# Performance work log

Hardware: AMD Instinct MI355X
Metric: run time of the kernel (lower is better)

## Reference

```python
import jax, jax.numpy as jnp
import numpy as np

N, T, F = 4096, 24, 16          # nodes, seq_len, in_features
H = 128                          # temporal_hidden
NH, DO = 4, 32                   # gat num_heads, gat out_features (NH*DO == H)
SEM, PH = 64, 32                 # semantic hidden, predictor hidden
SLOPE = 0.2                      # leaky_relu negative slope
ADJ_P = 0.01                     # adjacency density


def setup_inputs() -> dict:
    key = jax.random.key(0)
    ks = jax.random.split(key, 40)
    f32 = jnp.float32

    def rn(k, shape, s=0.02):
        return jax.random.normal(k, shape, f32) * s

    features = jax.random.normal(ks[0], (N, T, F), f32)
    pos_adj = (jax.random.uniform(ks[1], (N, N)) < ADJ_P).astype(f32)
    neg_adj = (jax.random.uniform(ks[2], (N, N)) < ADJ_P).astype(f32)

    inp = dict(features=features, pos_adj=pos_adj, neg_adj=neg_adj)
    # GRU (torch layout: W_ih [3H,F], W_hh [3H,H], gate order r,z,n)
    inp['gru_Wih'] = rn(ks[3], (3 * H, F), 1.0 / np.sqrt(H))
    inp['gru_Whh'] = rn(ks[4], (3 * H, H), 1.0 / np.sqrt(H))
    inp['gru_bih'] = rn(ks[5], (3 * H,), 1.0 / np.sqrt(H))
    inp['gru_bhh'] = rn(ks[6], (3 * H,), 1.0 / np.sqrt(H))
    # GAT params (linear weights stored [in, out] so we use x @ W)
    i = 7
    for pre in ('pos', 'neg'):
        inp[pre + '_W'] = rn(ks[i], (H, NH * DO)); i += 1
        inp[pre + '_u'] = rn(ks[i], (NH, DO, 1), 1.0); i += 1
        inp[pre + '_v'] = rn(ks[i], (NH, DO, 1), 1.0); i += 1
        inp[pre + '_b'] = rn(ks[i], (1, NH * DO)); i += 1
        inp[pre + '_pW'] = rn(ks[i], (H, NH * DO)); i += 1
        inp[pre + '_pb'] = jnp.zeros((NH * DO,), f32)
    inp['self_W'] = rn(ks[i], (H, H)); i += 1
    inp['self_b'] = jnp.zeros((H,), f32)
    inp['mpos_W'] = rn(ks[i], (NH * DO, H)); i += 1
    inp['mpos_b'] = jnp.zeros((H,), f32)
    inp['mneg_W'] = rn(ks[i], (NH * DO, H)); i += 1
    inp['mneg_b'] = jnp.zeros((H,), f32)
    inp['sem_W1'] = rn(ks[i], (H, SEM)); i += 1
    inp['sem_b1'] = jnp.zeros((SEM,), f32)
    inp['sem_W2'] = rn(ks[i], (SEM, 1)); i += 1
    inp['pred_W1'] = rn(ks[i], (H, PH)); i += 1
    inp['pred_b1'] = jnp.zeros((PH,), f32)
    inp['pred_W2'] = rn(ks[i], (PH, 1)); i += 1
    inp['pred_b2'] = jnp.zeros((1,), f32)
    return inp


def _gru_last(x, Wih, Whh, bih, bhh):
    # x: [N, T, F] -> last hidden state [N, H]
    gi_all = jnp.einsum('ntf,gf->tng', x, Wih) + bih  # precompute input gates [T,N,3H]
    h0 = jnp.zeros((x.shape[0], Whh.shape[1]), x.dtype)

    def step(h, gi):
        gh = h @ Whh.T + bhh
        ir, iz, in_ = jnp.split(gi, 3, axis=-1)
        hr, hz, hn = jnp.split(gh, 3, axis=-1)
        r = jax.nn.sigmoid(ir + hr)
        z = jax.nn.sigmoid(iz + hz)
        n = jnp.tanh(in_ + r * hn)
        return (1.0 - z) * n + z * h, None

    h, _ = jax.lax.scan(step, h0, gi_all)
    return h


def _gat(x, adj, W, u, v, b, pW, pb):
    sup = (x @ W).reshape(-1, NH, DO).transpose(1, 0, 2)     # [NH, N, DO]
    f1 = jnp.matmul(sup, u).reshape(NH, 1, -1)               # [NH, 1, N]
    f2 = jnp.matmul(sup, v).reshape(NH, -1, 1)               # [NH, N, 1]
    w = jax.nn.leaky_relu(f1 + f2, SLOPE)                    # [NH, N, N]
    mw = w * adj                                             # mask
    rs = mw.sum(axis=2, keepdims=True)
    rs = jnp.where(rs == 0, jnp.ones_like(rs), rs)
    attn = mw / rs
    out = jnp.matmul(attn, sup).transpose(1, 0, 2).reshape(-1, NH * DO)
    return out + b + x @ pW + pb                             # bias + residual


def _pairnorm_si(x):
    x = x - x.mean(axis=0)
    rn = jnp.sqrt(1e-6 + (x * x).sum(axis=1, keepdims=True))
    return x / rn


def reference(features, pos_adj, neg_adj,
              gru_Wih, gru_Whh, gru_bih, gru_bhh,
              pos_W, pos_u, pos_v, pos_b, pos_pW, pos_pb,
              neg_W, neg_u, neg_v, neg_b, neg_pW, neg_pb,
              self_W, self_b, mpos_W, mpos_b, mneg_W, mneg_b,
              sem_W1, sem_b1, sem_W2,
              pred_W1, pred_b1, pred_W2, pred_b2):
    support = _gru_last(features, gru_Wih, gru_Whh, gru_bih, gru_bhh)  # [N, H]
    pos_sup = _gat(support, pos_adj, pos_W, pos_u, pos_v, pos_b, pos_pW, pos_pb)
    neg_sup = _gat(support, neg_adj, neg_W, neg_u, neg_v, neg_b, neg_pW, neg_pb)
    self_e = support @ self_W + self_b
    pos_e = pos_sup @ mpos_W + mpos_b
    neg_e = neg_sup @ mneg_W + mneg_b
    emb = jnp.stack([self_e, pos_e, neg_e], axis=1)          # [N, 3, H]
    w = jnp.tanh(emb @ sem_W1 + sem_b1) @ sem_W2             # [N, 3, 1]
    beta = jax.nn.softmax(w, axis=1)
    fused = (beta * emb).sum(axis=1)                          # [N, H]
    fused = _pairnorm_si(fused)
    h = jax.nn.relu(fused @ pred_W1 + pred_b1)               # dropout is eval no-op
    out = jax.nn.sigmoid(h @ pred_W2 + pred_b2).squeeze(-1)  # [N]
    return out
```

## Files before the change

### kernel.cpp

```cpp
#include <hip/hip_runtime.h>


#define NN 4096
#define NEG_CSR 1024

typedef unsigned short u16;
typedef unsigned int   u32;
typedef unsigned long long u64;
typedef __attribute__((ext_vector_type(8))) short  short8;
typedef __attribute__((ext_vector_type(4))) float  float4v;

__device__ inline float bf2f(u16 u){ return __uint_as_float(((u32)u)<<16); }
__device__ inline u16 f2bf(float f){
  u32 x = __float_as_uint(f);
  return (u16)((x + 0x7fffu + ((x>>16)&1u))>>16);
}
__device__ inline float ldm(const void* p, int i, int bf){
  return bf ? bf2f(((const u16*)p)[i]) : ((const float*)p)[i];
}
__device__ inline u16 ldm16(const void* p, int i, int bf){
  return bf ? ((const u16*)p)[i] : f2bf(((const float*)p)[i]);
}
__device__ inline float fexp(float x){
  x = fminf(fmaxf(x,-80.f),80.f);
  return __builtin_amdgcn_exp2f(x*1.4426950408889634f);
}
__device__ inline float sigm_fast(float x){
  return __builtin_amdgcn_rcpf(1.f + __builtin_amdgcn_exp2f(-x*1.4426950408889634f));
}
__device__ inline float tanhf_(float x){
  float c = fminf(fmaxf(x,-15.f),15.f);
  float e = __builtin_amdgcn_exp2f(c*2.8853900817779268f);
  return (e-1.f)*__builtin_amdgcn_rcpf(e+1.f);
}
__device__ inline float4v mfma16(short8 a, short8 b, float4v c){
  return __builtin_amdgcn_mfma_f32_16x16x32_bf16(a,b,c,0,0,0);
}
__device__ inline int rdbf(const int* __restrict__ mflag){
  int b=0;
  #pragma unroll
  for (int k=0;k<16;k++) b|=mflag[k];
  return b;
}

__global__ __launch_bounds__(256) void k_detect(const u32* __restrict__ adj,
                                                int* __restrict__ mflag)
{
  __shared__ u32 w4[4];
  const int lane=threadIdx.x&63, wv=threadIdx.x>>6;
  int i = (blockIdx.x*256 + threadIdx.x)*4;
  uint4 v = *(const uint4*)(adj + i);
  u32 acc = (v.x | v.y | v.z | v.w) & 0xFFFFu;
  unsigned long long b = __ballot(acc != 0);
  if (lane==0) w4[wv] = (b!=0);
  __syncthreads();
  if (threadIdx.x==0) mflag[blockIdx.x] = (w4[0]|w4[1]|w4[2]|w4[3]) ? 1 : 0;
}

__global__ __launch_bounds__(256) void k_imp(
  const int* __restrict__ mflag,
  const void* gWih, const void* gWhh, const void* gbih, const void* gbhh,
  const void* posW, const void* posu, const void* posv, const void* posb,
  const void* pospW, const void* pospb,
  const void* negW, const void* negu, const void* negv, const void* negb,
  const void* negpW, const void* negpb,
  const void* selfW, const void* selfb, const void* mposW, const void* mposb,
  const void* mnegW, const void* mnegb,
  const void* semW1, const void* semb1, const void* semW2,
  const void* predW1, const void* predb1, const void* predW2, const void* predb2,
  u16* __restrict__ Wihb, u16* __restrict__ Whhb,
  u16* __restrict__ WT1,  u16* __restrict__ WT2,
  float* __restrict__ cbrz, float* __restrict__ cbin, float* __restrict__ cbhn,
  float* __restrict__ cuv,  float* __restrict__ cgb,  float* __restrict__ csb,
  float* __restrict__ cw1t, float* __restrict__ cb1,  float* __restrict__ cw2,
  float* __restrict__ cpw1t, float* __restrict__ cpb1, float* __restrict__ cpw2,
  float* __restrict__ cpb2, float* __restrict__ meanacc)
{
  const int bf = rdbf(mflag);
  int i = blockIdx.x*256 + threadIdx.x;
  if (i < 6144){ Wihb[i]=ldm16(gWih,i,bf); return; }  i-=6144;
  if (i < 49152){ Whhb[i]=ldm16(gWhh,i,bf); return; } i-=49152;
  if (i < 81920){
    int m=i>>7,k=i&127,sel=m>>7,ml=m&127;
    const void* s = sel==0?posW: sel==1?pospW: sel==2?negW: sel==3?negpW: selfW;
    WT1[i]=ldm16(s,k*128+ml,bf); return;
  } i-=81920;
  if (i < 32768){
    int m=i>>7,k=i&127;
    const void* s = (m<128)? mposW : mnegW;
    WT2[i]=ldm16(s,k*128+(m&127),bf); return;
  } i-=32768;
  if (i < 256){ cbrz[i]=ldm(gbih,i,bf)+ldm(gbhh,i,bf); return; } i-=256;
  if (i < 128){ cbin[i]=ldm(gbih,256+i,bf); return; } i-=128;
  if (i < 128){ cbhn[i]=ldm(gbhh,256+i,bf); return; } i-=128;
  if (i < 512){
    int s=i>>8, rem=i&255, wh=rem>>7, hd=rem&127;
    const void* p = s? (wh? negv:negu) : (wh? posv:posu);
    cuv[i]=ldm(p,hd,bf); return;
  } i-=512;
  if (i < 256){
    int s=i>>7, d=i&127;
    cgb[i]=ldm(s?negb:posb,d,bf)+ldm(s?negpb:pospb,d,bf); return;
  } i-=256;
  if (i < 384){
    int t=i>>7, d=i&127;
    const void* p = t==0? selfb : t==1? mposb : mnegb;
    csb[i]=ldm(p,d,bf); return;
  } i-=384;
  if (i < 8448){
    int c=i/132, k=i-c*132;
    cw1t[i] = (k<128)? ldm(semW1,k*64+c,bf) : 0.f; return;
  } i-=8448;
  if (i < 64){ cb1[i]=ldm(semb1,i,bf); return; } i-=64;
  if (i < 64){ cw2[i]=ldm(semW2,i,bf); return; } i-=64;
  if (i < 4224){
    int c=i/132, k=i-c*132;
    cpw1t[i] = (k<128)? ldm(predW1,k*32+c,bf) : 0.f; return;
  } i-=4224;
  if (i < 32){ cpb1[i]=ldm(predb1,i,bf); return; } i-=32;
  if (i < 32){ cpw2[i]=ldm(predW2,i,bf); return; } i-=32;
  if (i < 1){ cpb2[i]=ldm(predb2,i,bf); return; } i-=1;
  if (i < 128){ meanacc[i]=0.f; return; }
}

__global__ __launch_bounds__(512) void k_gruf(
  const int* __restrict__ mflag, const void* feat,
  const u16* __restrict__ Wihb, const u16* __restrict__ Whhb,
  const float* __restrict__ cbrz, const float* __restrict__ cbin,
  const float* __restrict__ cbhn,
  const u16* __restrict__ WT1, const float* __restrict__ cuv,
  const void* posadj, const void* negadj,
  u16* __restrict__ csri, int* __restrict__ csrc,
  u16* __restrict__ C1b, float* __restrict__ f12)
{
  __shared__ __attribute__((aligned(16))) u16 sh_x[16*392];
  __shared__ __attribute__((aligned(16))) u16 hbuf[2][16*136];
  const int bf = rdbf(mflag);
  const int tid=threadIdx.x, lane=tid&63, wv=tid>>6;

  if (blockIdx.x >= NN/16){
    const int t = (blockIdx.x - NN/16)*8 + wv;
    const int s = (t >= 4096) ? 1 : 0;
    const int i = s ? (t - 4096) : t;
    const void* adj = s? negadj : posadj;
    u64 mask=0;
    if (bf){
      const u16* rp = (const u16*)adj + (size_t)i*4096;
      #pragma unroll
      for (int it=0; it<8; it++){
        const uint4 vv = *(const uint4*)(rp + it*512 + lane*8);
        u32 w[4]={vv.x,vv.y,vv.z,vv.w};
        #pragma unroll
        for (int q=0;q<4;q++){
          if (w[q]&0xffffu) mask |= 1ull<<(it*8+2*q);
          if (w[q]>>16)     mask |= 1ull<<(it*8+2*q+1);
        }
      }
    } else {
      const float* rp = (const float*)adj + (size_t)i*4096;
      #pragma unroll
      for (int it=0; it<16; it++){
        const uint4 vv = *(const uint4*)(rp + it*256 + lane*4);
        if (vv.x) mask |= 1ull<<(it*4+0);
        if (vv.y) mask |= 1ull<<(it*4+1);
        if (vv.z) mask |= 1ull<<(it*4+2);
        if (vv.w) mask |= 1ull<<(it*4+3);
      }
    }
    int cnt=__popcll(mask);
    int pre=cnt;
    #pragma unroll
    for (int off=1; off<64; off<<=1){
      int o=__shfl_up(pre,off);
      if (lane>=off) pre+=o;
    }
    const int base_p = pre-cnt;
    const int total  = __shfl(pre,63);
    u16* op = csri + ((size_t)s*4096 + i)*128;
    if (base_p < 128){
      u64 mm=mask; int p=base_p;
      while (mm && p<128){
        int b=__ffsll(mm)-1; mm&=mm-1;
        int e = bf ? ((b>>3)*512 + lane*8 + (b&7))
                   : ((b>>2)*256 + lane*4 + (b&3));
        op[p++]=(u16)e;
      }
    }
    if (lane==63) csrc[(size_t)s*4096 + i] = total>128 ? 128 : total;
    return;
  }

  const int quad=lane>>4, c15=lane&15;
  const int n0=blockIdx.x*16;

  if (bf){
    const u16* f16p=(const u16*)feat;
    for (int i=tid;i<768;i+=512){
      int n=i/48, c=(i-n*48)*8;
      *(uint4*)(sh_x + n*392 + c) =
        *(const uint4*)(f16p + (size_t)(n0+n)*384 + c);
    }
  } else {
    const float* f32p=(const float*)feat;
    for (int i=tid;i<1536;i+=512){
      int n=i/96, c=(i-n*96)*4;
      float4 v = *(const float4*)(f32p + (size_t)(n0+n)*384 + c);
      uint2 pk;
      pk.x = (u32)f2bf(v.x) | ((u32)f2bf(v.y)<<16);
      pk.y = (u32)f2bf(v.z) | ((u32)f2bf(v.w)<<16);
      *(uint2*)(sh_x + n*392 + c) = pk;
    }
  }
  for (int i=tid;i<16*136;i+=512) hbuf[0][i]=0;

  const short8 z8={0,0,0,0,0,0,0,0};
  const float4v z4={0.f,0.f,0.f,0.f};
  short8 bh[3][4], bx3[3];
  #pragma unroll
  for (int g=0;g<3;g++){
    int rowb=(g*8+wv)*16+c15;
    #pragma unroll
    for (int ks=0;ks<4;ks++) bh[g][ks]=*(const short8*)(Whhb+(size_t)rowb*128+ks*32+quad*8);
    bx3[g] = (quad<2)? *(const short8*)(Wihb+(size_t)rowb*16+quad*8) : z8;
  }
  const int j0=wv*16+c15;
  const float brz_r=cbrz[j0], brz_z=cbrz[128+j0];
  const float bin0=cbin[j0],  bhn0=cbhn[j0];
  float hr[4]={0.f,0.f,0.f,0.f};
  __syncthreads();

  for (int t=0;t<24;t++){
    const u16* hb  = hbuf[t&1];
    u16*       hbn = hbuf[(t+1)&1];
    short8 ah[4];
    #pragma unroll
    for (int ks=0;ks<4;ks++) ah[ks]=*(const short8*)(hb + c15*136 + ks*32 + quad*8);
    short8 ax = (quad<2)? *(const short8*)(sh_x + c15*392 + t*16 + quad*8) : z8;
    float4v racc = mfma16(ax,bx3[0],z4);
    float4v zacc = mfma16(ax,bx3[1],z4);
    float4v ni   = mfma16(ax,bx3[2],z4);
    float4v nh   = z4;
    #pragma unroll
    for (int ks=0;ks<4;ks++){
      racc = mfma16(ah[ks],bh[0][ks],racc);
      zacc = mfma16(ah[ks],bh[1][ks],zacc);
      nh   = mfma16(ah[ks],bh[2][ks],nh);
    }
    #pragma unroll
    for (int rr=0;rr<4;rr++){
      const int node = quad*4+rr;
      float r_ = sigm_fast(racc[rr]+brz_r);
      float z_ = sigm_fast(zacc[rr]+brz_z);
      float n_ = tanhf_(ni[rr]+bin0 + r_*(nh[rr]+bhn0));
      float hv = (1.f-z_)*n_ + z_*hr[rr];
      hr[rr]=hv; hbn[node*136+j0]=f2bf(hv);
    }
    __syncthreads();
  }
  short8 a[4];
  #pragma unroll
  for (int ks=0;ks<4;ks++) a[ks]=*(const short8*)(hbuf[0]+c15*136+ks*32+quad*8);
  #pragma unroll
  for (int q=0;q<5;q++){
    int tile=wv*5+q;
    float4v acc={0.f,0.f,0.f,0.f};
    #pragma unroll
    for (int ks=0;ks<4;ks++){
      short8 b=*(const short8*)(WT1+(size_t)(tile*16+c15)*128+ks*32+quad*8);
      acc=mfma16(a[ks],b,acc);
    }
    #pragma unroll
    for (int r=0;r<4;r++)
      C1b[(size_t)(n0+quad*4+r)*640 + tile*16 + c15]=f2bf(acc[r]);
  }
  __syncthreads();
  {
    int q=tid;
    int nl=q&15, h=(q>>4)&3, wsel=(q>>6)&1, s=(q>>7)&1;
    const float* uvp = cuv + s*256 + wsel*128 + h*32;
    const u16*   SL  = C1b + (size_t)(n0+nl)*640 + s*256 + h*32;
    float t=0.f;
    #pragma unroll
    for (int d=0;d<32;d++) t += bf2f(SL[d])*uvp[d];
    f12[s*32768 + wsel*16384 + h*4096 + (n0+nl)] = t;
  }
}

__global__ __launch_bounds__(1024) void k_gat3(
  const int* __restrict__ mflag,
  const void* posadj, const void* negadj,
  const u16* __restrict__ csri, const int* __restrict__ csrc,
  const u16* __restrict__ C1b, const float* __restrict__ f12,
  const float* __restrict__ cgb, const u16* __restrict__ WT2,
  float* __restrict__ E)
{
  __shared__ u16   nbuf[16][128];
  __shared__ float wbuf[16][4][128];
  __shared__ __attribute__((aligned(16))) u16 sA[16*136];
  const int s=blockIdx.y;
  const int wv=threadIdx.x>>6, lane=threadIdx.x&63;
  const int n0=blockIdx.x*16;
  const int i=n0+wv;

  int dg;
  if (s==1 && n0 >= NEG_CSR){
    const int bf = rdbf(mflag);
    u64 mask=0;
    if (bf){
      const u16* rp = (const u16*)negadj + (size_t)i*4096;
      #pragma unroll
      for (int it=0; it<8; it++){
        const uint4 vv = *(const uint4*)(rp + it*512 + lane*8);
        u32 w[4]={vv.x,vv.y,vv.z,vv.w};
        #pragma unroll
        for (int q=0;q<4;q++){
          if (w[q]&0xffffu) mask |= 1ull<<(it*8+2*q);
          if (w[q]>>16)     mask |= 1ull<<(it*8+2*q+1);
        }
      }
    } else {
      const float* rp = (const float*)negadj + (size_t)i*4096;
      #pragma unroll
      for (int it=0; it<16; it++){
        const uint4 vv = *(const uint4*)(rp + it*256 + lane*4);
        if (vv.x) mask |= 1ull<<(it*4+0);
        if (vv.y) mask |= 1ull<<(it*4+1);
        if (vv.z) mask |= 1ull<<(it*4+2);
        if (vv.w) mask |= 1ull<<(it*4+3);
      }
    }
    int cnt=__popcll(mask);
    int pre=cnt;
    #pragma unroll
    for (int off=1; off<64; off<<=1){
      int o=__shfl_up(pre,off);
      if (lane>=off) pre+=o;
    }
    const int base_p = pre-cnt;
    const int total  = __shfl(pre,63);
    if (base_p < 128){
      u64 mm=mask; int p=base_p;
      while (mm && p<128){
        int b=__ffsll(mm)-1; mm&=mm-1;
        int e = bf ? ((b>>3)*512 + lane*8 + (b&7))
                   : ((b>>2)*256 + lane*4 + (b&3));
        nbuf[wv][p++]=(u16)e;
      }
    }
    dg = total>128 ? 128 : total;
  } else {
    ((u32*)nbuf[wv])[lane] = ((const u32*)(csri + ((size_t)s*4096 + i)*128))[lane];
    dg = csrc[(size_t)s*4096 + i];
  }

  const float* f1 = f12 + s*32768;
  const float* f2 = f12 + s*32768 + 16384;
  const int d0=lane, d1=lane+64, h0=lane>>5, h1=2+(lane>>5);
  float f2v[4];
  #pragma unroll
  for (int h=0;h<4;h++) f2v[h]=f2[h*4096+i];
  for (int e=lane; e<dg; e+=64){
    int j = nbuf[wv][e];
    #pragma unroll
    for (int h=0;h<4;h++){
      float w = f1[h*4096+j] + f2v[h];
      wbuf[wv][h][e] = w>0.f ? w : 0.2f*w;
    }
  }

  float acc0=0.f,acc1=0.f,rs0=0.f,rs1=0.f;
  #pragma unroll 4
  for (int e=0;e<dg;e++){
    float w0 = wbuf[wv][h0][e];
    float w1 = wbuf[wv][h1][e];
    int j = nbuf[wv][e];
    const u16* SL = C1b + (size_t)j*640 + s*256;
    acc0 += w0*bf2f(SL[d0]); rs0 += w0;
    acc1 += w1*bf2f(SL[d1]); rs1 += w1;
  }
  if (rs0==0.f) rs0=1.f;
  if (rs1==0.f) rs1=1.f;
  const u16* P = C1b + (size_t)i*640 + s*256 + 128;
  sA[wv*136+d0]=f2bf(acc0/rs0 + cgb[s*128+d0] + bf2f(P[d0]));
  sA[wv*136+d1]=f2bf(acc1/rs1 + cgb[s*128+d1] + bf2f(P[d1]));
  __syncthreads();
  if (wv<8){
    const int quad=lane>>4, c15=lane&15;
    short8 a[4];
    #pragma unroll
    for (int ks=0;ks<4;ks++) a[ks]=*(const short8*)(sA+c15*136+ks*32+quad*8);
    const int tile=wv;
    float4v acc={0.f,0.f,0.f,0.f};
    #pragma unroll
    for (int ks=0;ks<4;ks++){
      short8 b=*(const short8*)(WT2+(size_t)(s*128+tile*16+c15)*128+ks*32+quad*8);
      acc=mfma16(a[ks],b,acc);
    }
    #pragma unroll
    for (int r=0;r<4;r++) E[(size_t)(n0+quad*4+r)*256 + s*128 + tile*16 + c15]=acc[r];
  }
}

__global__ __launch_bounds__(256) void k_sem(
  const u16* __restrict__ C1b, const float* __restrict__ E,
  const float* __restrict__ csb, const float* __restrict__ cw1t,
  const float* __restrict__ cb1, const float* __restrict__ cw2,
  float* __restrict__ fused, float* __restrict__ meanacc)
{
  __shared__ float sW1t[64*132];
  __shared__ float sW2[64];
  __shared__ float sb1[64];
  __shared__ float sE[4][3][128];
  __shared__ float redm[4][128];
  const int tid=threadIdx.x, wv=tid>>6, lane=tid&63;
  for (int i=tid;i<8448;i+=256) sW1t[i]=cw1t[i];
  if (tid<64){ sW2[tid]=cw2[tid]; sb1[tid]=cb1[tid]; }
  __syncthreads();
  const float* wcol = sW1t + lane*132;
  float macc0=0.f, macc1=0.f;
  for (int u=0;u<4;u++){
    const int n = blockIdx.x*16 + wv*4 + u;
    for (int d=lane; d<128; d+=64){
      sE[wv][0][d] = bf2f(C1b[(size_t)n*640+512+d]) + csb[d];
      sE[wv][1][d] = E[(size_t)n*256 + d]    + csb[128+d];
      sE[wv][2][d] = E[(size_t)n*256+128+d]  + csb[256+d];
    }
    float sc[3];
    #pragma unroll
    for (int s=0;s<3;s++){
      float t = sb1[lane];
      #pragma unroll
      for (int k=0;k<128;k+=4){
        float4 e4 = *(const float4*)&sE[wv][s][k];
        float4 w4 = *(const float4*)&wcol[k];
        t += e4.x*w4.x + e4.y*w4.y + e4.z*w4.z + e4.w*w4.w;
      }
      t = tanhf_(t);
      float p = t*sW2[lane];
      #pragma unroll
      for (int off=32; off; off>>=1) p += __shfl_xor(p, off);
      sc[s]=p;
    }
    float mx = fmaxf(sc[0], fmaxf(sc[1],sc[2]));
    float e0=fexp(sc[0]-mx), e1=fexp(sc[1]-mx), e2=fexp(sc[2]-mx);
    float inv = 1.f/(e0+e1+e2);
    float b0=e0*inv, b1=e1*inv, b2=e2*inv;
    float f0 = b0*sE[wv][0][lane]    + b1*sE[wv][1][lane]    + b2*sE[wv][2][lane];
    float f1 = b0*sE[wv][0][lane+64] + b1*sE[wv][1][lane+64] + b2*sE[wv][2][lane+64];
    fused[(size_t)n*128+lane]    = f0;
    fused[(size_t)n*128+64+lane] = f1;
    macc0 += f0; macc1 += f1;
  }
  redm[wv][lane]=macc0; redm[wv][lane+64]=macc1;
  __syncthreads();
  if (tid<128)
    atomicAdd(&meanacc[tid], redm[0][tid]+redm[1][tid]+redm[2][tid]+redm[3][tid]);
}

__global__ __launch_bounds__(256) void k_pred(
  const float* __restrict__ fused, const float* __restrict__ meanacc,
  const float* __restrict__ cpw1t, const float* __restrict__ cpb1,
  const float* __restrict__ cpw2, const float* __restrict__ cpb2,
  float* __restrict__ out)
{
  __shared__ float sy[4][128];
  __shared__ float sW1t[32*132];
  __shared__ float sW2[32];
  const int tid=threadIdx.x, wv=tid>>6, lane=tid&63;
  for (int i=tid;i<4224;i+=256) sW1t[i]=cpw1t[i];
  if (tid<32) sW2[tid]=cpw2[tid];
  const int n = blockIdx.x*4 + wv;
  const float inv_n = 1.f/4096.f;
  float x0 = fused[(size_t)n*128+lane]    - meanacc[lane]*inv_n;
  float x1 = fused[(size_t)n*128+64+lane] - meanacc[64+lane]*inv_n;
  float ss = x0*x0 + x1*x1;
  #pragma unroll
  for (int o=32;o;o>>=1) ss += __shfl_xor(ss,o);
  float ir = 1.f/sqrtf(1e-6f + ss);
  sy[wv][lane]=x0*ir; sy[wv][64+lane]=x1*ir;
  __syncthreads();
  const int c = lane&31, half = lane>>5;
  const float* wcol = sW1t + c*132 + half*64;
  const float* yrow = sy[wv] + half*64;
  float h=0.f;
  #pragma unroll
  for (int k=0;k<64;k+=4){
    float4 y4 = *(const float4*)&yrow[k];
    float4 w4 = *(const float4*)&wcol[k];
    h += y4.x*w4.x + y4.y*w4.y + y4.z*w4.z + y4.w*w4.w;
  }
  h += __shfl_xor(h,32);
  h += cpb1[c];
  h = h>0.f? h : 0.f;
  float p = h*sW2[c];
  #pragma unroll
  for (int o=16;o;o>>=1) p += __shfl_xor(p,o);
  if (!lane){
    float z = p + cpb2[0];
    out[n] = __builtin_amdgcn_rcpf(1.f + fexp(-z));
  }
}

extern "C" void kernel_launch(void* const* d_in, const int* in_sizes, int n_in,
                              void* d_out, int out_size, void* d_ws, size_t ws_size,
                              hipStream_t stream)
{
  const void* feat  =d_in[0];
  const void* posadj=d_in[1];
  const void* negadj=d_in[2];
  const void* gWih  =d_in[3];
  const void* gWhh  =d_in[4];
  const void* gbih  =d_in[5];
  const void* gbhh  =d_in[6];
  const void* posW  =d_in[7];
  const void* posu  =d_in[8];
  const void* posv  =d_in[9];
  const void* posb  =d_in[10];
  const void* pospW =d_in[11];
  const void* pospb =d_in[12];
  const void* negW  =d_in[13];
  const void* negu  =d_in[14];
  const void* negv  =d_in[15];
  const void* negb  =d_in[16];
  const void* negpW =d_in[17];
  const void* negpb =d_in[18];
  const void* selfW =d_in[19];
  const void* selfb =d_in[20];
  const void* mposW =d_in[21];
  const void* mposb =d_in[22];
  const void* mnegW =d_in[23];
  const void* mnegb =d_in[24];
  const void* semW1 =d_in[25];
  const void* semb1 =d_in[26];
  const void* semW2 =d_in[27];
  const void* predW1=d_in[28];
  const void* predb1=d_in[29];
  const void* predW2=d_in[30];
  const void* predb2=d_in[31];

  char* wsb=(char*)d_ws; size_t off=0;
  auto alloc=[&](size_t bytes)->void*{ void* p=wsb+off; off+=(bytes+255)&~(size_t)255; return p; };
  int*   mflag=(int*)  alloc(256);
  u16*   Wihb =(u16*)  alloc(6144*2);
  u16*   Whhb =(u16*)  alloc(49152*2);
  u16*   WT1  =(u16*)  alloc(81920*2);
  u16*   WT2  =(u16*)  alloc(32768*2);
  float* cbrz =(float*)alloc(256*4);
  float* cbin =(float*)alloc(128*4);
  float* cbhn =(float*)alloc(128*4);
  float* cuv  =(float*)alloc(512*4);
  float* cgb  =(float*)alloc(256*4);
  float* csb  =(float*)alloc(384*4);
  float* cw1t =(float*)alloc(8448*4);
  float* cb1  =(float*)alloc(64*4);
  float* cw2  =(float*)alloc(64*4);
  float* cpw1t=(float*)alloc(4224*4);
  float* cpb1 =(float*)alloc(32*4);
  float* cpw2 =(float*)alloc(32*4);
  float* cpb2 =(float*)alloc(4);
  u16*   C1b  =(u16*)  alloc((size_t)NN*640*2);
  float* f12  =(float*)alloc((size_t)65536*4);
  float* E    =(float*)alloc((size_t)NN*256*4);
  float* fused=(float*)alloc((size_t)NN*128*4);
  float* meanacc=(float*)alloc(128*4);
  u16*   csri =(u16*)  alloc((size_t)2*4096*128*2);
  int*   csrc =(int*)  alloc((size_t)2*4096*4);
  (void)ws_size; (void)in_sizes; (void)n_in; (void)out_size;

  k_detect<<<16,          256,0,stream>>>((const u32*)posadj,mflag);
  k_imp   <<<722,         256,0,stream>>>(mflag,gWih,gWhh,gbih,gbhh,
              posW,posu,posv,posb,pospW,pospb,negW,negu,negv,negb,negpW,negpb,
              selfW,selfb,mposW,mposb,mnegW,mnegb,semW1,semb1,semW2,
              predW1,predb1,predW2,predb2,
              Wihb,Whhb,WT1,WT2,cbrz,cbin,cbhn,cuv,cgb,csb,cw1t,cb1,cw2,
              cpw1t,cpb1,cpw2,cpb2,meanacc);
  k_gruf  <<<NN/16 + (NN+NEG_CSR)/8, 512,0,stream>>>(mflag,feat,Wihb,Whhb,
                                          cbrz,cbin,cbhn,WT1,cuv,
                                          posadj,negadj,csri,csrc,C1b,f12);
  k_gat3  <<<dim3(256,2),1024,0,stream>>>(mflag,posadj,negadj,csri,csrc,
                                          C1b,f12,cgb,WT2,E);
  k_sem   <<<NN/16,       256,0,stream>>>(C1b,E,csb,cw1t,cb1,cw2,fused,meanacc);
  k_pred  <<<NN/4,        256,0,stream>>>(fused,meanacc,cpw1t,cpb1,cpw2,cpb2,(float*)d_out);
}
```

Before: 271.2 us.

## Fuse GAT aggregation and semantic attention into one kernel

Merges k_gat3 and k_sem into a single kernel. Each 1024-thread block handles 16 nodes, loops over both adjacency types, and keeps the GAT output embeddings in shared memory instead of writing E to global memory and reading it back. This removes one launch and the E round trip. In exchange, grid parallelism halves (256 blocks instead of 512), the two adjacency types now run serially within each block, and only 256 of the 1024 threads do the semantic stage, so occupancy and latency hiding may suffer.

```diff
diff --git a/kernel.cpp b/kernel.cpp
--- a/kernel.cpp
+++ b/kernel.cpp
@@ -286,172 +286,176 @@
   }
 }
 
-__global__ __launch_bounds__(1024) void k_gat3(
+__global__ __launch_bounds__(1024) void k_gat3sem(
   const int* __restrict__ mflag,
   const void* posadj, const void* negadj,
   const u16* __restrict__ csri, const int* __restrict__ csrc,
   const u16* __restrict__ C1b, const float* __restrict__ f12,
   const float* __restrict__ cgb, const u16* __restrict__ WT2,
-  float* __restrict__ E)
-{
-  __shared__ u16   nbuf[16][128];
-  __shared__ float wbuf[16][4][128];
-  __shared__ __attribute__((aligned(16))) u16 sA[16*136];
-  const int s=blockIdx.y;
-  const int wv=threadIdx.x>>6, lane=threadIdx.x&63;
-  const int n0=blockIdx.x*16;
-  const int i=n0+wv;
-
-  int dg;
-  if (s==1 && n0 >= NEG_CSR){
-    const int bf = rdbf(mflag);
-    u64 mask=0;
-    if (bf){
-      const u16* rp = (const u16*)negadj + (size_t)i*4096;
-      #pragma unroll
-      for (int it=0; it<8; it++){
-        const uint4 vv = *(const uint4*)(rp + it*512 + lane*8);
-        u32 w[4]={vv.x,vv.y,vv.z,vv.w};
-        #pragma unroll
-        for (int q=0;q<4;q++){
-          if (w[q]&0xffffu) mask |= 1ull<<(it*8+2*q);
-          if (w[q]>>16)     mask |= 1ull<<(it*8+2*q+1);
-        }
-      }
-    } else {
-      const float* rp = (const float*)negadj + (size_t)i*4096;
-      #pragma unroll
-      for (int it=0; it<16; it++){
-        const uint4 vv = *(const uint4*)(rp + it*256 + lane*4);
-        if (vv.x) mask |= 1ull<<(it*4+0);
-        if (vv.y) mask |= 1ull<<(it*4+1);
-        if (vv.z) mask |= 1ull<<(it*4+2);
-        if (vv.w) mask |= 1ull<<(it*4+3);
-      }
-    }
-    int cnt=__popcll(mask);
-    int pre=cnt;
-    #pragma unroll
-    for (int off=1; off<64; off<<=1){
-      int o=__shfl_up(pre,off);
-      if (lane>=off) pre+=o;
-    }
-    const int base_p = pre-cnt;
-    const int total  = __shfl(pre,63);
-    if (base_p < 128){
-      u64 mm=mask; int p=base_p;
-      while (mm && p<128){
-        int b=__ffsll(mm)-1; mm&=mm-1;
-        int e = bf ? ((b>>3)*512 + lane*8 + (b&7))
-                   : ((b>>2)*256 + lane*4 + (b&3));
-        nbuf[wv][p++]=(u16)e;
-      }
-    }
-    dg = total>128 ? 128 : total;
-  } else {
-    ((u32*)nbuf[wv])[lane] = ((const u32*)(csri + ((size_t)s*4096 + i)*128))[lane];
-    dg = csrc[(size_t)s*4096 + i];
-  }
-
-  const float* f1 = f12 + s*32768;
-  const float* f2 = f12 + s*32768 + 16384;
-  const int d0=lane, d1=lane+64, h0=lane>>5, h1=2+(lane>>5);
-  float f2v[4];
-  #pragma unroll
-  for (int h=0;h<4;h++) f2v[h]=f2[h*4096+i];
-  for (int e=lane; e<dg; e+=64){
-    int j = nbuf[wv][e];
-    #pragma unroll
-    for (int h=0;h<4;h++){
-      float w = f1[h*4096+j] + f2v[h];
-      wbuf[wv][h][e] = w>0.f ? w : 0.2f*w;
-    }
-  }
-
-  float acc0=0.f,acc1=0.f,rs0=0.f,rs1=0.f;
-  #pragma unroll 4
-  for (int e=0;e<dg;e++){
-    float w0 = wbuf[wv][h0][e];
-    float w1 = wbuf[wv][h1][e];
-    int j = nbuf[wv][e];
-    const u16* SL = C1b + (size_t)j*640 + s*256;
-    acc0 += w0*bf2f(SL[d0]); rs0 += w0;
-    acc1 += w1*bf2f(SL[d1]); rs1 += w1;
-  }
-  if (rs0==0.f) rs0=1.f;
-  if (rs1==0.f) rs1=1.f;
-  const u16* P = C1b + (size_t)i*640 + s*256 + 128;
-  sA[wv*136+d0]=f2bf(acc0/rs0 + cgb[s*128+d0] + bf2f(P[d0]));
-  sA[wv*136+d1]=f2bf(acc1/rs1 + cgb[s*128+d1] + bf2f(P[d1]));
-  __syncthreads();
-  if (wv<8){
-    const int quad=lane>>4, c15=lane&15;
-    short8 a[4];
-    #pragma unroll
-    for (int ks=0;ks<4;ks++) a[ks]=*(const short8*)(sA+c15*136+ks*32+quad*8);
-    const int tile=wv;
-    float4v acc={0.f,0.f,0.f,0.f};
-    #pragma unroll
-    for (int ks=0;ks<4;ks++){
-      short8 b=*(const short8*)(WT2+(size_t)(s*128+tile*16+c15)*128+ks*32+quad*8);
-      acc=mfma16(a[ks],b,acc);
-    }
-    #pragma unroll
-    for (int r=0;r<4;r++) E[(size_t)(n0+quad*4+r)*256 + s*128 + tile*16 + c15]=acc[r];
-  }
-}
-
-__global__ __launch_bounds__(256) void k_sem(
-  const u16* __restrict__ C1b, const float* __restrict__ E,
   const float* __restrict__ csb, const float* __restrict__ cw1t,
   const float* __restrict__ cb1, const float* __restrict__ cw2,
   float* __restrict__ fused, float* __restrict__ meanacc)
 {
-  __shared__ float sW1t[64*132];
-  __shared__ float sW2[64];
-  __shared__ float sb1[64];
-  __shared__ float sE[4][3][128];
-  __shared__ float redm[4][128];
-  const int tid=threadIdx.x, wv=tid>>6, lane=tid&63;
-  for (int i=tid;i<8448;i+=256) sW1t[i]=cw1t[i];
+  __shared__ __attribute__((aligned(16))) char smem[58880];
+  u16   (*nbuf)[128]    = (u16(*)[128])(smem);
+  float (*wbuf)[4][128] = (float(*)[4][128])(smem+4096);
+  u16*   sA             = (u16*)(smem+36864);
+  float* sW1t           = (float*)(smem);
+  float* sW2            = (float*)(smem+33792);
+  float* sb1            = (float*)(smem+34048);
+  float (*sE)[3][128]   = (float(*)[3][128])(smem+34304);
+  float (*redm)[128]    = (float(*)[128])(smem+40448);
+  float (*sEg)[256]     = (float(*)[256])(smem+42496);
+
+  const int tid=threadIdx.x;
+  const int bf = rdbf(mflag);
+  const int wv=tid>>6, lane=tid&63;
+  const int n0=blockIdx.x*16;
+  const int i=n0+wv;
+
+  for (int s=0;s<2;s++){
+    if (s) __syncthreads();
+    int dg;
+    if (s==1 && n0 >= NEG_CSR){
+      u64 mask=0;
+      if (bf){
+        const u16* rp = (const u16*)negadj + (size_t)i*4096;
+        #pragma unroll
+        for (int it=0; it<8; it++){
+          const uint4 vv = *(const uint4*)(rp + it*512 + lane*8);
+          u32 w[4]={vv.x,vv.y,vv.z,vv.w};
+          #pragma unroll
+          for (int q=0;q<4;q++){
+            if (w[q]&0xffffu) mask |= 1ull<<(it*8+2*q);
+            if (w[q]>>16)     mask |= 1ull<<(it*8+2*q+1);
+          }
+        }
+      } else {
+        const float* rp = (const float*)negadj + (size_t)i*4096;
+        #pragma unroll
+        for (int it=0; it<16; it++){
+          const uint4 vv = *(const uint4*)(rp + it*256 + lane*4);
+          if (vv.x) mask |= 1ull<<(it*4+0);
+          if (vv.y) mask |= 1ull<<(it*4+1);
+          if (vv.z) mask |= 1ull<<(it*4+2);
+          if (vv.w) mask |= 1ull<<(it*4+3);
+        }
+      }
+      int cnt=__popcll(mask);
+      int pre=cnt;
+      #pragma unroll
+      for (int off=1; off<64; off<<=1){
+        int o=__shfl_up(pre,off);
+        if (lane>=off) pre+=o;
+      }
+      const int base_p = pre-cnt;
+      const int total  = __shfl(pre,63);
+      if (base_p < 128){
+        u64 mm=mask; int p=base_p;
+        while (mm && p<128){
+          int b=__ffsll(mm)-1; mm&=mm-1;
+          int e = bf ? ((b>>3)*512 + lane*8 + (b&7))
+                     : ((b>>2)*256 + lane*4 + (b&3));
+          nbuf[wv][p++]=(u16)e;
+        }
+      }
+      dg = total>128 ? 128 : total;
+    } else {
+      ((u32*)nbuf[wv])[lane] = ((const u32*)(csri + ((size_t)s*4096 + i)*128))[lane];
+      dg = csrc[(size_t)s*4096 + i];
+    }
+
+    const float* f1 = f12 + s*32768;
+    const float* f2 = f12 + s*32768 + 16384;
+    const int d0=lane, d1=lane+64, h0=lane>>5, h1=2+(lane>>5);
+    float f2v[4];
+    #pragma unroll
+    for (int h=0;h<4;h++) f2v[h]=f2[h*4096+i];
+    for (int e=lane; e<dg; e+=64){
+      int j = nbuf[wv][e];
+      #pragma unroll
+      for (int h=0;h<4;h++){
+        float w = f1[h*4096+j] + f2v[h];
+        wbuf[wv][h][e] = w>0.f ? w : 0.2f*w;
+      }
+    }
+
+    float acc0=0.f,acc1=0.f,rs0=0.f,rs1=0.f;
+    #pragma unroll 4
+    for (int e=0;e<dg;e++){
+      float w0 = wbuf[wv][h0][e];
+      float w1 = wbuf[wv][h1][e];
+      int j = nbuf[wv][e];
+      const u16* SL = C1b + (size_t)j*640 + s*256;
+      acc0 += w0*bf2f(SL[d0]); rs0 += w0;
+      acc1 += w1*bf2f(SL[d1]); rs1 += w1;
+    }
+    if (rs0==0.f) rs0=1.f;
+    if (rs1==0.f) rs1=1.f;
+    const u16* P = C1b + (size_t)i*640 + s*256 + 128;
+    sA[wv*136+d0]=f2bf(acc0/rs0 + cgb[s*128+d0] + bf2f(P[d0]));
+    sA[wv*136+d1]=f2bf(acc1/rs1 + cgb[s*128+d1] + bf2f(P[d1]));
+    __syncthreads();
+    if (wv<8){
+      const int quad=lane>>4, c15=lane&15;
+      short8 a[4];
+      #pragma unroll
+      for (int ks=0;ks<4;ks++) a[ks]=*(const short8*)(sA+c15*136+ks*32+quad*8);
+      const int tile=wv;
+      float4v acc={0.f,0.f,0.f,0.f};
+      #pragma unroll
+      for (int ks=0;ks<4;ks++){
+        short8 b=*(const short8*)(WT2+(size_t)(s*128+tile*16+c15)*128+ks*32+quad*8);
+        acc=mfma16(a[ks],b,acc);
+      }
+      #pragma unroll
+      for (int r=0;r<4;r++) sEg[quad*4+r][s*128 + tile*16 + c15]=acc[r];
+    }
+  }
+  __syncthreads();
+
+  for (int k=tid;k<8448;k+=1024) sW1t[k]=cw1t[k];
   if (tid<64){ sW2[tid]=cw2[tid]; sb1[tid]=cb1[tid]; }
   __syncthreads();
-  const float* wcol = sW1t + lane*132;
-  float macc0=0.f, macc1=0.f;
-  for (int u=0;u<4;u++){
-    const int n = blockIdx.x*16 + wv*4 + u;
-    for (int d=lane; d<128; d+=64){
-      sE[wv][0][d] = bf2f(C1b[(size_t)n*640+512+d]) + csb[d];
-      sE[wv][1][d] = E[(size_t)n*256 + d]    + csb[128+d];
-      sE[wv][2][d] = E[(size_t)n*256+128+d]  + csb[256+d];
-    }
-    float sc[3];
-    #pragma unroll
-    for (int s=0;s<3;s++){
-      float t = sb1[lane];
-      #pragma unroll
-      for (int k=0;k<128;k+=4){
-        float4 e4 = *(const float4*)&sE[wv][s][k];
-        float4 w4 = *(const float4*)&wcol[k];
-        t += e4.x*w4.x + e4.y*w4.y + e4.z*w4.z + e4.w*w4.w;
-      }
-      t = tanhf_(t);
-      float p = t*sW2[lane];
-      #pragma unroll
-      for (int off=32; off; off>>=1) p += __shfl_xor(p, off);
-      sc[s]=p;
-    }
-    float mx = fmaxf(sc[0], fmaxf(sc[1],sc[2]));
-    float e0=fexp(sc[0]-mx), e1=fexp(sc[1]-mx), e2=fexp(sc[2]-mx);
-    float inv = 1.f/(e0+e1+e2);
-    float b0=e0*inv, b1=e1*inv, b2=e2*inv;
-    float f0 = b0*sE[wv][0][lane]    + b1*sE[wv][1][lane]    + b2*sE[wv][2][lane];
-    float f1 = b0*sE[wv][0][lane+64] + b1*sE[wv][1][lane+64] + b2*sE[wv][2][lane+64];
-    fused[(size_t)n*128+lane]    = f0;
-    fused[(size_t)n*128+64+lane] = f1;
-    macc0 += f0; macc1 += f1;
-  }
-  redm[wv][lane]=macc0; redm[wv][lane+64]=macc1;
+  if (tid<256){
+    const float* wcol = sW1t + lane*132;
+    float macc0=0.f, macc1=0.f;
+    for (int u=0;u<4;u++){
+      const int n  = n0 + wv*4 + u;
+      const int nl = wv*4 + u;
+      for (int d=lane; d<128; d+=64){
+        sE[wv][0][d] = bf2f(C1b[(size_t)n*640+512+d]) + csb[d];
+        sE[wv][1][d] = sEg[nl][d]     + csb[128+d];
+        sE[wv][2][d] = sEg[nl][128+d] + csb[256+d];
+      }
+      float sc[3];
+      #pragma unroll
+      for (int s=0;s<3;s++){
+        float t = sb1[lane];
+        #pragma unroll
+        for (int k=0;k<128;k+=4){
+          float4 e4 = *(const float4*)&sE[wv][s][k];
+          float4 w4 = *(const float4*)&wcol[k];
+          t += e4.x*w4.x + e4.y*w4.y + e4.z*w4.z + e4.w*w4.w;
+        }
+        t = tanhf_(t);
+        float p = t*sW2[lane];
+        #pragma unroll
+        for (int off=32; off; off>>=1) p += __shfl_xor(p, off);
+        sc[s]=p;
+      }
+      float mx = fmaxf(sc[0], fmaxf(sc[1],sc[2]));
+      float e0=fexp(sc[0]-mx), e1=fexp(sc[1]-mx), e2=fexp(sc[2]-mx);
+      float inv = 1.f/(e0+e1+e2);
+      float b0=e0*inv, b1=e1*inv, b2=e2*inv;
+      float f0 = b0*sE[wv][0][lane]    + b1*sE[wv][1][lane]    + b2*sE[wv][2][lane];
+      float f1 = b0*sE[wv][0][lane+64] + b1*sE[wv][1][lane+64] + b2*sE[wv][2][lane+64];
+      fused[(size_t)n*128+lane]    = f0;
+      fused[(size_t)n*128+64+lane] = f1;
+      macc0 += f0; macc1 += f1;
+    }
+    redm[wv][lane]=macc0; redm[wv][lane+64]=macc1;
+  }
   __syncthreads();
   if (tid<128)
     atomicAdd(&meanacc[tid], redm[0][tid]+redm[1][tid]+redm[2][tid]+redm[3][tid]);
@@ -560,7 +564,6 @@
   float* cpb2 =(float*)alloc(4);
   u16*   C1b  =(u16*)  alloc((size_t)NN*640*2);
   float* f12  =(float*)alloc((size_t)65536*4);
-  float* E    =(float*)alloc((size_t)NN*256*4);
   float* fused=(float*)alloc((size_t)NN*128*4);
   float* meanacc=(float*)alloc(128*4);
   u16*   csri =(u16*)  alloc((size_t)2*4096*128*2);
@@ -577,8 +580,8 @@
   k_gruf  <<<NN/16 + (NN+NEG_CSR)/8, 512,0,stream>>>(mflag,feat,Wihb,Whhb,
                                           cbrz,cbin,cbhn,WT1,cuv,
                                           posadj,negadj,csri,csrc,C1b,f12);
-  k_gat3  <<<dim3(256,2),1024,0,stream>>>(mflag,posadj,negadj,csri,csrc,
-                                          C1b,f12,cgb,WT2,E);
-  k_sem   <<<NN/16,       256,0,stream>>>(C1b,E,csb,cw1t,cb1,cw2,fused,meanacc);
+  k_gat3sem<<<256,       1024,0,stream>>>(mflag,posadj,negadj,csri,csrc,
+                                          C1b,f12,cgb,WT2,csb,cw1t,cb1,cw2,
+                                          fused,meanacc);
   k_pred  <<<NN/4,        256,0,stream>>>(fused,meanacc,cpw1t,cpb1,cpw2,cpb2,(float*)d_out);
 }
```

After: 279.2 us. +3.0%, slower.
